# Performance work log

Hardware: AMD Instinct MI355X
Metric: run time of the kernel (lower is better)

Reference implementation:

```python
import jax, jax.numpy as jnp
import numpy as np

EMBED_DIM = 1024
NUM_HEADS = 16
FFN_DIM = 4096
N_QUBITS = 8
LN_EPS = 1e-5


def _layernorm(x, g, b):
    mu = jnp.mean(x, axis=-1, keepdims=True)
    var = jnp.mean(jnp.square(x - mu), axis=-1, keepdims=True)
    return (x - mu) * jax.lax.rsqrt(var + LN_EPS) * g + b


def setup_inputs() -> dict:
    key = jax.random.key(0)
    ks = jax.random.split(key, 12)
    E, F_, Q = EMBED_DIM, FFN_DIM, N_QUBITS
    s = 1.0 / np.sqrt(E)
    return {
        "x": jax.random.normal(ks[0], (4, 2048, E), dtype=jnp.float32),
        "wq": jax.random.normal(ks[1], (E, E), dtype=jnp.float32) * s,
        "wk": jax.random.normal(ks[2], (E, E), dtype=jnp.float32) * s,
        "wv": jax.random.normal(ks[3], (E, E), dtype=jnp.float32) * s,
        "wo": jax.random.normal(ks[4], (E, E), dtype=jnp.float32) * s,
        "theta": jax.random.normal(ks[5], (Q,), dtype=jnp.float32),
        "w1": jax.random.normal(ks[6], (Q, F_), dtype=jnp.float32) * (1.0 / np.sqrt(Q)),
        "w2": jax.random.normal(ks[7], (F_, E), dtype=jnp.float32) * (1.0 / np.sqrt(F_)),
        "ln1_g": jnp.ones((E,), dtype=jnp.float32),
        "ln1_b": jnp.zeros((E,), dtype=jnp.float32),
        "ln2_g": jnp.ones((E,), dtype=jnp.float32),
        "ln2_b": jnp.zeros((E,), dtype=jnp.float32),
    }


def reference(x, wq, wk, wv, wo, theta, w1, w2, ln1_g, ln1_b, ln2_g, ln2_b):
    B, S, E = x.shape
    H, Dk = NUM_HEADS, E // NUM_HEADS
    # ---- multi-head attention ----
    q = (x @ wq).reshape(B, S, H, Dk).transpose(0, 2, 1, 3)  # [B,H,S,Dk]
    k = (x @ wk).reshape(B, S, H, Dk).transpose(0, 2, 1, 3)
    v = (x @ wv).reshape(B, S, H, Dk).transpose(0, 2, 1, 3)
    scores = jnp.einsum("bhsd,bhtd->bhst", q, k) / np.sqrt(Dk)
    attn = jax.nn.softmax(scores, axis=-1)
    ctx = jnp.einsum("bhst,bhtd->bhsd", attn, v)
    ctx = ctx.transpose(0, 2, 1, 3).reshape(B, S, E)
    attn_out = ctx @ wo
    x1 = _layernorm(x + attn_out, ln1_g, ln1_b)
    # ---- quantum FFN ----
    # Per qubit w: |0> -> RX(x1_w) -> RX(x1_w) -> RX(theta_w); <Z> = cos(2*x1_w + theta_w)
    q_out = jnp.cos(2.0 * x1[..., :N_QUBITS] + theta)  # [B,S,Q]
    ffn_out = jax.nn.relu(q_out @ w1) @ w2  # [B,S,E]
    return _layernorm(x1 + ffn_out, ln2_g, ln2_b)
```

## Files before the change

### kernel.cpp

```cpp
#include <hip/hip_runtime.h>
#include <hip/hip_bf16.h>


typedef __attribute__((ext_vector_type(8))) short bf16x8;
typedef __attribute__((ext_vector_type(16))) float f32x16;
typedef __attribute__((ext_vector_type(4))) unsigned short u16x4;

__device__ __forceinline__ unsigned short f2bf(float f) {
  union { float f; unsigned int u; } v; v.f = f;
  return (unsigned short)((v.u + 0x7FFFu + ((v.u >> 16) & 1u)) >> 16);
}
__device__ __forceinline__ float bf2f(unsigned short h) {
  union { unsigned int u; float f; } v; v.u = ((unsigned int)h) << 16;
  return v.f;
}
__device__ __forceinline__ f32x16 mfma32(bf16x8 a, bf16x8 b, f32x16 c) {
  return __builtin_amdgcn_mfma_f32_32x32x16_bf16(a, b, c, 0, 0, 0);
}
__device__ __forceinline__ void lds_cp16(const void* g, void* l) {
  __builtin_amdgcn_global_load_lds(
      (const __attribute__((address_space(1))) unsigned int*)g,
      (__attribute__((address_space(3))) unsigned int*)l, 16, 0, 0);
}

#define QG_CONV(P, FC0, FC1)                                                  \
  {                                                                           \
    int x0a, x0b, x1a, x1b, x2a, x2b, x3a, x3b;                               \
    asm("v_cvt_pk_bf16_f32 %0, %1, %2" : "=v"(x0a) : "v"(P[0]),  "v"(P[1]));  \
    asm("v_cvt_pk_bf16_f32 %0, %1, %2" : "=v"(x0b) : "v"(P[2]),  "v"(P[3]));  \
    asm("v_cvt_pk_bf16_f32 %0, %1, %2" : "=v"(x1a) : "v"(P[4]),  "v"(P[5]));  \
    asm("v_cvt_pk_bf16_f32 %0, %1, %2" : "=v"(x1b) : "v"(P[6]),  "v"(P[7]));  \
    asm("v_cvt_pk_bf16_f32 %0, %1, %2" : "=v"(x2a) : "v"(P[8]),  "v"(P[9]));  \
    asm("v_cvt_pk_bf16_f32 %0, %1, %2" : "=v"(x2b) : "v"(P[10]), "v"(P[11])); \
    asm("v_cvt_pk_bf16_f32 %0, %1, %2" : "=v"(x3a) : "v"(P[12]), "v"(P[13])); \
    asm("v_cvt_pk_bf16_f32 %0, %1, %2" : "=v"(x3b) : "v"(P[14]), "v"(P[15])); \
    asm("v_permlane32_swap_b32 %0, %1" : "+v"(x0a), "+v"(x1a));               \
    asm("v_permlane32_swap_b32 %0, %1" : "+v"(x0b), "+v"(x1b));               \
    asm("v_permlane32_swap_b32 %0, %1" : "+v"(x2a), "+v"(x3a));               \
    asm("v_permlane32_swap_b32 %0, %1" : "+v"(x2b), "+v"(x3b));               \
    union { int u[4]; bf16x8 v; } f0_, f1_;                                   \
    f0_.u[0] = x0a; f0_.u[1] = x0b; f0_.u[2] = x1a; f0_.u[3] = x1b;           \
    f1_.u[0] = x2a; f1_.u[1] = x2b; f1_.u[2] = x3a; f1_.u[3] = x3b;           \
    FC0 = f0_.v; FC1 = f1_.v;                                                 \
  }

__global__ __launch_bounds__(256) void cast_x_kernel(const float* __restrict__ in,
                                                     unsigned short* __restrict__ out,
                                                     int n4) {
  int i = blockIdx.x * 256 + threadIdx.x;
  if (i >= n4) return;
  float4 v = ((const float4*)in)[i];
  u16x4 o = { f2bf(v.x), f2bf(v.y), f2bf(v.z), f2bf(v.w) };
  ((u16x4*)out)[i] = o;
}

__global__ __launch_bounds__(256) void transpose_cast_kernel(const float* __restrict__ in,
                                                             unsigned short* __restrict__ out,
                                                             int K, int N) {
  __shared__ float tile[32][33];
  const int n0 = blockIdx.x * 32, k0 = blockIdx.y * 32;
  const int tx = threadIdx.x, ty = threadIdx.y;
#pragma unroll
  for (int i = 0; i < 32; i += 8)
    tile[ty + i][tx] = in[(long)(k0 + ty + i) * N + n0 + tx];
  __syncthreads();
#pragma unroll
  for (int i = 0; i < 32; i += 8)
    out[(long)(n0 + ty + i) * K + k0 + tx] = f2bf(tile[tx][ty + i]);
}

__global__ __launch_bounds__(256) void w1t_kernel(const float* __restrict__ w1,
                                                  unsigned short* __restrict__ w1t) {
  const int f = blockIdx.x * 256 + threadIdx.x;
  unsigned short v[8];
#pragma unroll
  for (int q = 0; q < 8; q++) v[q] = f2bf(w1[q * 4096 + f]);
  *(u16x4*)(w1t + f * 8)     = (u16x4){v[0], v[1], v[2], v[3]};
  *(u16x4*)(w1t + f * 8 + 4) = (u16x4){v[4], v[5], v[6], v[7]};
}

__global__ __launch_bounds__(256) void vt_kernel(const unsigned short* __restrict__ qkv,
                                                 unsigned short* __restrict__ vT) {
  __shared__ unsigned short tile[32][34];
  const int t0 = blockIdx.x * 32, d0 = blockIdx.y * 32, bh = blockIdx.z;
  const int b = bh >> 4, h = bh & 15;
  const int tx = threadIdx.x, ty = threadIdx.y;
  const unsigned short* src = qkv + (long)(b * 2048 + t0) * 3072 + 2048 + h * 64 + d0;
#pragma unroll
  for (int i = 0; i < 32; i += 8)
    tile[ty + i][tx] = src[(long)(ty + i) * 3072 + tx];
  __syncthreads();
  unsigned short* dst = vT + ((long)bh * 64 + d0) * 2048 + t0;
#pragma unroll
  for (int i = 0; i < 32; i += 8)
    dst[(long)(ty + i) * 2048 + tx] = tile[tx][ty + i];
}

template<int EPI>
__global__ __launch_bounds__(256) void gemm_bt3(const unsigned short* __restrict__ A,
                                                const unsigned short* __restrict__ BT,
                                                void* __restrict__ Cv,
                                                int M, int N, int K) {
  __shared__ __align__(16) unsigned char smem[2][32768];
  const int tid = threadIdx.x;
  const int l = tid & 63, w = tid >> 6;
  const int l32 = l & 31, h32 = l >> 5;
  const int wrm = (w >> 1) * 64;
  const int wrn = (w & 1) * 64;

  const int nx = gridDim.x;
  const int nwg = nx * gridDim.y;
  const int orig = blockIdx.y * nx + blockIdx.x;
  const int chunk = nwg >> 3;
  const int logical = (orig & 7) * chunk + (orig >> 3);
  const long m0 = (long)(logical / nx) * 128;
  const long n0 = (long)(logical % nx) * 128;

  const unsigned short* gp[8];
  unsigned ldsoff[8];
#pragma unroll
  for (int i = 0; i < 8; i++) {
    const int c = (i & 3) * 256 + tid;
    const int r = c >> 3, k8 = c & 7;
    if (i < 4) {
      gp[i] = A + (m0 + r) * (long)K + (k8 ^ (r & 7)) * 8;
      ldsoff[i] = (unsigned)c * 16;
    } else {
      gp[i] = BT + (n0 + r) * (long)K + (k8 ^ (r & 7)) * 8;
      ldsoff[i] = 16384u + (unsigned)c * 16;
    }
  }

  f32x16 acc[2][2];
#pragma unroll
  for (int mf = 0; mf < 2; mf++)
#pragma unroll
    for (int nf = 0; nf < 2; nf++)
#pragma unroll
      for (int e = 0; e < 16; e++) acc[mf][nf][e] = 0.f;

  const int NT = K >> 6;
#define STAGE(bf, t)                                                    \
  do {                                                                  \
    unsigned char* _d = &smem[bf][0];                                   \
    const long _ko = (long)(t) * 64;                                    \
    _Pragma("unroll")                                                   \
    for (int _i = 0; _i < 8; _i++)                                      \
      lds_cp16(gp[_i] + _ko, _d + ldsoff[_i]);                          \
  } while (0)

  STAGE(0, 0);
  int cur = 0;
  for (int t = 0; t < NT; t++) {
    if (t + 1 < NT) {
      STAGE(cur ^ 1, t + 1);
      asm volatile("s_waitcnt vmcnt(8)" ::: "memory");
    } else {
      asm volatile("s_waitcnt vmcnt(0)" ::: "memory");
    }
    __builtin_amdgcn_sched_barrier(0);
    __builtin_amdgcn_s_barrier();
    __builtin_amdgcn_sched_barrier(0);

    const unsigned char* bufA = &smem[cur][0];
    const unsigned char* bufB = &smem[cur][16384];
    bf16x8 af[2][4], bfr[2][4];
#pragma unroll
    for (int mf = 0; mf < 2; mf++) {
      const int r = wrm + mf * 32 + l32;
#pragma unroll
      for (int ks = 0; ks < 4; ks++)
        af[mf][ks] = *(const bf16x8*)(bufA + r * 128 + (((ks * 2 + h32) ^ (r & 7)) * 16));
    }
#pragma unroll
    for (int nf = 0; nf < 2; nf++) {
      const int r = wrn + nf * 32 + l32;
#pragma unroll
      for (int ks = 0; ks < 4; ks++)
        bfr[nf][ks] = *(const bf16x8*)(bufB + r * 128 + (((ks * 2 + h32) ^ (r & 7)) * 16));
    }
    __builtin_amdgcn_s_setprio(1);
#pragma unroll
    for (int ks = 0; ks < 4; ks++)
#pragma unroll
      for (int mf = 0; mf < 2; mf++)
#pragma unroll
        for (int nf = 0; nf < 2; nf++)
          acc[mf][nf] = mfma32(af[mf][ks], bfr[nf][ks], acc[mf][nf]);
    __builtin_amdgcn_s_setprio(0);
    __builtin_amdgcn_sched_barrier(0);
    __builtin_amdgcn_s_barrier();
    cur ^= 1;
  }
#undef STAGE

#pragma unroll
  for (int mf = 0; mf < 2; mf++)
#pragma unroll
    for (int nf = 0; nf < 2; nf++) {
      const long c0 = n0 + wrn + nf * 32 + l32;
#pragma unroll
      for (int reg = 0; reg < 16; reg++) {
        const long r0 = m0 + wrm + mf * 32 + (reg & 3) + 8 * (reg >> 2) + 4 * h32;
        if (EPI == 0) ((float*)Cv)[r0 * (long)N + c0] = acc[mf][nf][reg];
        else ((unsigned short*)Cv)[r0 * (long)N + c0] = f2bf(acc[mf][nf][reg]);
      }
    }
}

__global__ __launch_bounds__(512) void ffn_fused(const unsigned short* __restrict__ qo,
                                                 const unsigned short* __restrict__ w1t,
                                                 const unsigned short* __restrict__ BT,
                                                 float* __restrict__ Cp0,
                                                 float* __restrict__ Cp1,
                                                 int N, int K) {
  __shared__ __align__(16) unsigned char sm[2 * 16384 + 32768 + 4096];
  unsigned char* lsW = sm + 32768;
  unsigned char* lsQ = sm + 65536;
  const int tid = threadIdx.x;
  const int l = tid & 63, w = tid >> 6;
  const int l32 = l & 31, h32 = l >> 5;
  const int wrm = (w >> 1) * 64;
  const int wrn = (w & 1) * 64;

  const int nx = gridDim.x;
  const int nwg = nx * gridDim.y;
  const int orig = blockIdx.y * nx + blockIdx.x;
  const int chunk = nwg >> 3;
  const int logical = (orig & 7) * chunk + (orig >> 3);
  const long m0 = (long)(logical / nx) * 256;
  const long n0 = (long)(logical % nx) * 128;
  const int kz = blockIdx.z;
  const int NT = (K >> 6) >> 1;
  const int tbase = kz * NT;
  float* C = kz ? Cp1 : Cp0;

  const unsigned short* gpB[2];
  unsigned offB[2];
#pragma unroll
  for (int i = 0; i < 2; i++) {
    const int c = i * 512 + tid;
    const int r = c >> 3, k8 = c & 7;
    gpB[i] = BT + (n0 + r) * (long)K + (long)tbase * 64 + (k8 ^ (r & 7)) * 8;
    offB[i] = (unsigned)c * 16;
  }
  const unsigned short* w1base = w1t + (long)tbase * 64 * 8;

  const bf16x8 z8 = {0, 0, 0, 0, 0, 0, 0, 0};

#define STAGE_B(bf, t)                                                  \
  do {                                                                  \
    unsigned char* _d = sm + (bf) * 16384;                              \
    const long _ko = (long)(t) * 64;                                    \
    lds_cp16(gpB[0] + _ko, _d + offB[0]);                               \
    lds_cp16(gpB[1] + _ko, _d + offB[1]);                               \
  } while (0)
#define STAGE_W1(T)                                                     \
  lds_cp16(w1base + (long)((T) * 64 + l) * 8, lsW + ((unsigned)(T) << 10))

  STAGE_W1(0);
  STAGE_W1(1);
  if (w < 4) lds_cp16(qo + (m0 + w * 64 + l) * 8, lsQ + (unsigned)(w * 64) * 16);
  STAGE_B(0, 0);
  asm volatile("s_waitcnt vmcnt(0)" ::: "memory");
  __builtin_amdgcn_s_barrier();

  bf16x8 qof[2];
#pragma unroll
  for (int mf = 0; mf < 2; mf++)
    qof[mf] = (h32 == 0) ? *(const bf16x8*)(lsQ + (wrm + mf * 32 + l32) * 16) : z8;

  f32x16 zz;
#pragma unroll
  for (int e = 0; e < 16; e++) zz[e] = 0.f;
  f32x16 acc[2][2];
#pragma unroll
  for (int mf = 0; mf < 2; mf++)
#pragma unroll
    for (int nf = 0; nf < 2; nf++) acc[mf][nf] = zz;

  f32x16 hP0, hP1;
  {
    bf16x8 wf0 = (h32 == 0) ? *(const bf16x8*)(lsW + (0 + l32) * 16) : z8;
    bf16x8 wf1 = (h32 == 0) ? *(const bf16x8*)(lsW + (32 + l32) * 16) : z8;
    hP0 = mfma32(wf0, qof[0], zz);
    hP1 = mfma32(wf1, qof[0], zz);
  }

  int cur = 0;
  for (int t = 0; t < NT; t++) {
    if (t + 2 < NT) {
      STAGE_W1(t + 2);
      STAGE_B(cur ^ 1, t + 1);
      asm volatile("s_waitcnt vmcnt(3)" ::: "memory");
    } else if (t + 1 < NT) {
      STAGE_B(cur ^ 1, t + 1);
      asm volatile("s_waitcnt vmcnt(2)" ::: "memory");
    } else {
      asm volatile("s_waitcnt vmcnt(0)" ::: "memory");
    }
    __builtin_amdgcn_sched_barrier(0);
    __builtin_amdgcn_s_barrier();
    __builtin_amdgcn_sched_barrier(0);

    bf16x8 w1ft[2], w1fn[2];
#pragma unroll
    for (int tg = 0; tg < 2; tg++) {
      w1ft[tg] = (h32 == 0)
          ? *(const bf16x8*)(lsW + ((unsigned)t << 10) + (tg * 32 + l32) * 16) : z8;
      w1fn[tg] = (h32 == 0 && t + 1 < NT)
          ? *(const bf16x8*)(lsW + ((unsigned)(t + 1) << 10) + (tg * 32 + l32) * 16) : z8;
    }
    const unsigned char* bufB = sm + cur * 16384;
    bf16x8 bfr[2][4];
#pragma unroll
    for (int nf = 0; nf < 2; nf++) {
      const int r = wrn + nf * 32 + l32;
#pragma unroll
      for (int ks = 0; ks < 4; ks++)
        bfr[nf][ks] = *(const bf16x8*)(bufB + r * 128 + (((ks * 2 + h32) ^ (r & 7)) * 16));
    }

#pragma unroll
    for (int e = 0; e < 16; e++) {
      hP0[e] = fmaxf(hP0[e], 0.f);
      hP1[e] = fmaxf(hP1[e], 0.f);
    }
    bf16x8 a0, a1, a2, a3;
    QG_CONV(hP0, a0, a1)
    QG_CONV(hP1, a2, a3)
    __builtin_amdgcn_s_setprio(1);
    f32x16 hQ0 = mfma32(w1ft[0], qof[1], zz);
    f32x16 hQ1 = mfma32(w1ft[1], qof[1], zz);
    acc[0][0] = mfma32(a0, bfr[0][0], acc[0][0]);
    acc[0][0] = mfma32(a1, bfr[0][1], acc[0][0]);
    acc[0][0] = mfma32(a2, bfr[0][2], acc[0][0]);
    acc[0][0] = mfma32(a3, bfr[0][3], acc[0][0]);
    acc[0][1] = mfma32(a0, bfr[1][0], acc[0][1]);
    acc[0][1] = mfma32(a1, bfr[1][1], acc[0][1]);
    acc[0][1] = mfma32(a2, bfr[1][2], acc[0][1]);
    acc[0][1] = mfma32(a3, bfr[1][3], acc[0][1]);
    __builtin_amdgcn_s_setprio(0);

#pragma unroll
    for (int e = 0; e < 16; e++) {
      hQ0[e] = fmaxf(hQ0[e], 0.f);
      hQ1[e] = fmaxf(hQ1[e], 0.f);
    }
    bf16x8 b0, b1, b2, b3;
    QG_CONV(hQ0, b0, b1)
    QG_CONV(hQ1, b2, b3)
    __builtin_amdgcn_s_setprio(1);
    hP0 = mfma32(w1fn[0], qof[0], zz);
    hP1 = mfma32(w1fn[1], qof[0], zz);
    acc[1][0] = mfma32(b0, bfr[0][0], acc[1][0]);
    acc[1][0] = mfma32(b1, bfr[0][1], acc[1][0]);
    acc[1][0] = mfma32(b2, bfr[0][2], acc[1][0]);
    acc[1][0] = mfma32(b3, bfr[0][3], acc[1][0]);
    acc[1][1] = mfma32(b0, bfr[1][0], acc[1][1]);
    acc[1][1] = mfma32(b1, bfr[1][1], acc[1][1]);
    acc[1][1] = mfma32(b2, bfr[1][2], acc[1][1]);
    acc[1][1] = mfma32(b3, bfr[1][3], acc[1][1]);
    __builtin_amdgcn_s_setprio(0);

    __builtin_amdgcn_sched_barrier(0);
    __builtin_amdgcn_s_barrier();
    cur ^= 1;
  }
#undef STAGE_B
#undef STAGE_W1

#pragma unroll
  for (int mf = 0; mf < 2; mf++)
#pragma unroll
    for (int nf = 0; nf < 2; nf++) {
      const long c0 = n0 + wrn + nf * 32 + l32;
#pragma unroll
      for (int reg = 0; reg < 16; reg++) {
        const long r0 = m0 + wrm + mf * 32 + (reg & 3) + 8 * (reg >> 2) + 4 * h32;
        C[r0 * (long)N + c0] = acc[mf][nf][reg];
      }
    }
}

#define QG_BLOCK(P, LIP, FC0, FC1)                                            \
  {                                                                           \
    _Pragma("unroll")                                                         \
    for (int e = 0; e < 16; e++)                                              \
      asm("v_exp_f32 %0, %1" : "=v"(P[e]) : "v"(P[e]));                       \
    float s_ = 0.f;                                                           \
    _Pragma("unroll")                                                         \
    for (int e = 0; e < 16; e++) s_ += P[e];                                  \
    LIP += s_;                                                                \
    QG_CONV(P, FC0, FC1)                                                      \
  }

__global__ __launch_bounds__(256) void attn_kernel(const unsigned short* __restrict__ qkv,
                                                   const unsigned short* __restrict__ vT,
                                                   unsigned short* __restrict__ ctx) {
  __shared__ __align__(16) unsigned short lsK[64][72];
  __shared__ __align__(16) unsigned short lsV[64][72];

  const int tid = threadIdx.x;
  const int l = tid & 63, w = tid >> 6;
  const int l32 = l & 31, h32 = l >> 5;

  const int orig = blockIdx.x;
  const int logical = (orig & 7) * 64 + (orig >> 3);
  const int s0 = (logical & 7) * 256;
  const int bh = logical >> 3;
  const int b = bh >> 4, hh = bh & 15;

  const float QSC = 0.18033688f;
  const unsigned short* qg_base = qkv + (long)(b * 2048 + s0 + w * 64) * 3072 + hh * 64;
  bf16x8 qb0[4], qb1[4];
#pragma unroll
  for (int kc = 0; kc < 4; kc++) {
    bf16x8 t0v = *(const bf16x8*)(qg_base + (long)l32 * 3072 + kc * 16 + h32 * 8);
    bf16x8 t1v = *(const bf16x8*)(qg_base + (long)(32 + l32) * 3072 + kc * 16 + h32 * 8);
#pragma unroll
    for (int j = 0; j < 8; j++) {
      t0v[j] = (short)f2bf(bf2f((unsigned short)t0v[j]) * QSC);
      t1v[j] = (short)f2bf(bf2f((unsigned short)t1v[j]) * QSC);
    }
    qb0[kc] = t0v;
    qb1[kc] = t1v;
  }

  f32x16 oacc00, oacc01, oacc10, oacc11;
#pragma unroll
  for (int e = 0; e < 16; e++) {
    oacc00[e] = 0.f; oacc01[e] = 0.f; oacc10[e] = 0.f; oacc11[e] = 0.f;
  }
  float lip0 = 0.f, lip1 = 0.f;

  const int tr = tid >> 2;
  const int tc = (tid & 3) * 16;
  const unsigned short* kbase = qkv + (long)(b * 2048) * 3072 + 1024 + hh * 64;
  const unsigned short* vbase = vT + (long)bh * 64 * 2048;

  bf16x8 k0 = *(const bf16x8*)(kbase + (long)tr * 3072 + tc);
  bf16x8 k1 = *(const bf16x8*)(kbase + (long)tr * 3072 + tc + 8);
  bf16x8 v0 = *(const bf16x8*)(vbase + (long)tr * 2048 + tc);
  bf16x8 v1 = *(const bf16x8*)(vbase + (long)tr * 2048 + tc + 8);

  for (int t0 = 0; t0 < 2048; t0 += 64) {
    __syncthreads();
    *(bf16x8*)&lsK[tr][tc]     = k0;
    *(bf16x8*)&lsK[tr][tc + 8] = k1;
    *(bf16x8*)&lsV[tr][tc]     = v0;
    *(bf16x8*)&lsV[tr][tc + 8] = v1;
    __syncthreads();
    if (t0 + 64 < 2048) {
      k0 = *(const bf16x8*)(kbase + (long)(t0 + 64 + tr) * 3072 + tc);
      k1 = *(const bf16x8*)(kbase + (long)(t0 + 64 + tr) * 3072 + tc + 8);
      v0 = *(const bf16x8*)(vbase + (long)tr * 2048 + t0 + 64 + tc);
      v1 = *(const bf16x8*)(vbase + (long)tr * 2048 + t0 + 64 + tc + 8);
    }

#pragma unroll
    for (int tg = 0; tg < 2; tg++) {
      bf16x8 kb[4];
#pragma unroll
      for (int kc = 0; kc < 4; kc++)
        kb[kc] = *(const bf16x8*)&lsK[tg * 32 + l32][kc * 16 + h32 * 8];

      f32x16 p0, p1;
#pragma unroll
      for (int e = 0; e < 16; e++) { p0[e] = 0.f; p1[e] = 0.f; }
      __builtin_amdgcn_s_setprio(1);
#pragma unroll
      for (int kc = 0; kc < 4; kc++) {
        p0 = mfma32(kb[kc], qb0[kc], p0);
        p1 = mfma32(kb[kc], qb1[kc], p1);
      }
      __builtin_amdgcn_s_setprio(0);

      bf16x8 fA0, fA1, fB0, fB1;
      QG_BLOCK(p0, lip0, fA0, fA1)
      QG_BLOCK(p1, lip1, fB0, fB1)

      bf16x8 v00 = *(const bf16x8*)&lsV[l32][tg * 32 + h32 * 8];
      bf16x8 v01 = *(const bf16x8*)&lsV[l32][tg * 32 + 16 + h32 * 8];
      bf16x8 v10 = *(const bf16x8*)&lsV[32 + l32][tg * 32 + h32 * 8];
      bf16x8 v11 = *(const bf16x8*)&lsV[32 + l32][tg * 32 + 16 + h32 * 8];

      __builtin_amdgcn_s_setprio(1);
      oacc00 = mfma32(fA0, v00, oacc00);
      oacc00 = mfma32(fA1, v01, oacc00);
      oacc01 = mfma32(fA0, v10, oacc01);
      oacc01 = mfma32(fA1, v11, oacc01);
      oacc10 = mfma32(fB0, v00, oacc10);
      oacc10 = mfma32(fB1, v01, oacc10);
      oacc11 = mfma32(fB0, v10, oacc11);
      oacc11 = mfma32(fB1, v11, oacc11);
      __builtin_amdgcn_s_setprio(0);
    }
  }

  const float li0 = lip0 + __shfl_xor(lip0, 32);
  const float li1 = lip1 + __shfl_xor(lip1, 32);
  const float inv0 = 1.f / li0;
  const float inv1 = 1.f / li1;
  const long qrow0 = (long)(b * 2048 + s0 + w * 64);
  const int dcol = hh * 64 + l32;
#define STORE_QG(OA, OB, INV, QOFF)                                           \
  _Pragma("unroll")                                                           \
  for (int reg = 0; reg < 16; reg++) {                                        \
    const int rq = (reg & 3) + 8 * (reg >> 2) + 4 * h32;                      \
    const float iv = __shfl(INV, rq);                                         \
    const long q = qrow0 + (QOFF) + rq;                                       \
    ctx[q * 1024 + dcol]      = f2bf(OA[reg] * iv);                           \
    ctx[q * 1024 + dcol + 32] = f2bf(OB[reg] * iv);                           \
  }
  STORE_QG(oacc00, oacc01, inv0, 0)
  STORE_QG(oacc10, oacc11, inv1, 32)
#undef STORE_QG
}

template<bool QO, bool THREE>
__global__ __launch_bounds__(256) void ln_kernel(const float* __restrict__ ra,
                                                 const float* __restrict__ rb,
                                                 const float* __restrict__ rc,
                                                 const float* __restrict__ g,
                                                 const float* __restrict__ bb,
                                                 float* __restrict__ out,
                                                 unsigned short* __restrict__ qo,
                                                 const float* __restrict__ theta) {
  const int row = blockIdx.x;
  const int tid = threadIdx.x;
  const long base = (long)row * 1024 + tid * 4;
  float4 a = *(const float4*)(ra + base);
  float4 bv = *(const float4*)(rb + base);
  float4 r;
  r.x = a.x + bv.x; r.y = a.y + bv.y; r.z = a.z + bv.z; r.w = a.w + bv.w;
  if constexpr (THREE) {
    float4 c = *(const float4*)(rc + base);
    r.x += c.x; r.y += c.y; r.z += c.z; r.w += c.w;
  }
  float s  = r.x + r.y + r.z + r.w;
  float ss = r.x * r.x + r.y * r.y + r.z * r.z + r.w * r.w;
  for (int off = 32; off; off >>= 1) {
    s  += __shfl_down(s, off);
    ss += __shfl_down(ss, off);
  }
  __shared__ float red[4][2];
  const int wv = tid >> 6;
  if ((tid & 63) == 0) { red[wv][0] = s; red[wv][1] = ss; }
  __syncthreads();
  s  = red[0][0] + red[1][0] + red[2][0] + red[3][0];
  ss = red[0][1] + red[1][1] + red[2][1] + red[3][1];
  const float mu  = s * (1.f / 1024.f);
  const float var = ss * (1.f / 1024.f) - mu * mu;
  const float rsv = rsqrtf(var + 1e-5f);
  float4 gv  = *(const float4*)(g + tid * 4);
  float4 bbv = *(const float4*)(bb + tid * 4);
  float4 y;
  y.x = (r.x - mu) * rsv * gv.x + bbv.x;
  y.y = (r.y - mu) * rsv * gv.y + bbv.y;
  y.z = (r.z - mu) * rsv * gv.z + bbv.z;
  y.w = (r.w - mu) * rsv * gv.w + bbv.w;
  *(float4*)(out + base) = y;
  if constexpr (QO) {
    if (tid < 2) {
      float yv[4] = {y.x, y.y, y.z, y.w};
      u16x4 o;
#pragma unroll
      for (int c = 0; c < 4; c++)
        o[c] = f2bf(__cosf(2.f * yv[c] + theta[tid * 4 + c]));
      *(u16x4*)(qo + (long)row * 8 + tid * 4) = o;
    }
  }
}

extern "C" void kernel_launch(void* const* d_in, const int* in_sizes, int n_in,
                              void* d_out, int out_size, void* d_ws, size_t ws_size,
                              hipStream_t stream) {
  const float* x     = (const float*)d_in[0];
  const float* wq    = (const float*)d_in[1];
  const float* wk    = (const float*)d_in[2];
  const float* wv    = (const float*)d_in[3];
  const float* wo    = (const float*)d_in[4];
  const float* theta = (const float*)d_in[5];
  const float* w1    = (const float*)d_in[6];
  const float* w2    = (const float*)d_in[7];
  const float* g1    = (const float*)d_in[8];
  const float* b1    = (const float*)d_in[9];
  const float* g2    = (const float*)d_in[10];
  const float* b2    = (const float*)d_in[11];
  float* out = (float*)d_out;
  char* ws = (char*)d_ws;

  const long MB = 1 << 20;
  unsigned short* xb    = (unsigned short*)(ws);
  unsigned short* wqkvT = (unsigned short*)(ws + 16 * MB);
  unsigned short* woT   = (unsigned short*)(ws + 22 * MB);
  unsigned short* w2T   = (unsigned short*)(ws + 24 * MB);
  float*          x1    = (float*)(ws + 32 * MB);
  float*          fbuf  = (float*)(ws + 64 * MB);
  unsigned short* qkv   = (unsigned short*)(ws + 96 * MB);
  float*          fbuf2 = (float*)(ws + 96 * MB);
  unsigned short* vTb   = (unsigned short*)(ws + 144 * MB);
  unsigned short* qob   = (unsigned short*)(ws + 160 * MB);
  unsigned short* w1tb  = (unsigned short*)(ws + 160 * MB + 128 * 1024);
  unsigned short* ctx   = xb;

  cast_x_kernel<<<8192, 256, 0, stream>>>(x, xb, 8192 * 1024 / 4);
  dim3 tb(32, 8);
  transpose_cast_kernel<<<dim3(32, 32), tb, 0, stream>>>(wq, wqkvT, 1024, 1024);
  transpose_cast_kernel<<<dim3(32, 32), tb, 0, stream>>>(wk, wqkvT + 1024 * 1024, 1024, 1024);
  transpose_cast_kernel<<<dim3(32, 32), tb, 0, stream>>>(wv, wqkvT + 2048 * 1024, 1024, 1024);
  transpose_cast_kernel<<<dim3(32, 32), tb, 0, stream>>>(wo, woT, 1024, 1024);
  transpose_cast_kernel<<<dim3(32, 128), tb, 0, stream>>>(w2, w2T, 4096, 1024);
  w1t_kernel<<<16, 256, 0, stream>>>(w1, w1tb);

  gemm_bt3<1><<<dim3(24, 64), 256, 0, stream>>>(xb, wqkvT, qkv, 8192, 3072, 1024);

  vt_kernel<<<dim3(64, 2, 64), tb, 0, stream>>>(qkv, vTb);

  attn_kernel<<<512, 256, 0, stream>>>(qkv, vTb, ctx);

  gemm_bt3<0><<<dim3(8, 64), 256, 0, stream>>>(ctx, woT, fbuf, 8192, 1024, 1024);

  ln_kernel<true, false><<<8192, 256, 0, stream>>>(x, fbuf, nullptr, g1, b1, x1, qob, theta);

  ffn_fused<<<dim3(8, 32, 2), 512, 0, stream>>>(qob, w1tb, w2T, fbuf, fbuf2, 1024, 4096);

  ln_kernel<false, true><<<8192, 256, 0, stream>>>(x1, fbuf, fbuf2, g2, b2, out, nullptr, nullptr);
}
```

Before: 341.7 us.

## Merge weight-prep kernels into one launch and preload all W1 tiles upfront

```diff
diff --git a/kernel.cpp b/kernel.cpp
--- a/kernel.cpp
+++ b/kernel.cpp
@@ -54,29 +54,50 @@
   ((u16x4*)out)[i] = o;
 }
 
-__global__ __launch_bounds__(256) void transpose_cast_kernel(const float* __restrict__ in,
-                                                             unsigned short* __restrict__ out,
-                                                             int K, int N) {
+__global__ __launch_bounds__(256) void prep_weights(const float* __restrict__ wq,
+                                                    const float* __restrict__ wk,
+                                                    const float* __restrict__ wv,
+                                                    const float* __restrict__ wo,
+                                                    const float* __restrict__ w2,
+                                                    const float* __restrict__ w1,
+                                                    unsigned short* __restrict__ wqkvT,
+                                                    unsigned short* __restrict__ woT,
+                                                    unsigned short* __restrict__ w2T,
+                                                    unsigned short* __restrict__ w1t) {
   __shared__ float tile[32][33];
+  const int tx = threadIdx.x, ty = threadIdx.y;
+  const int z = blockIdx.z;
+
+  if (z == 0 && blockIdx.y >= 32) {
+    if (blockIdx.y < 48) {
+      const int f = (blockIdx.y - 32) * 256 + ty * 32 + tx;
+      unsigned short v[8];
+#pragma unroll
+      for (int q = 0; q < 8; q++) v[q] = f2bf(w1[q * 4096 + f]);
+      *(u16x4*)(w1t + f * 8)     = (u16x4){v[0], v[1], v[2], v[3]};
+      *(u16x4*)(w1t + f * 8 + 4) = (u16x4){v[4], v[5], v[6], v[7]};
+    }
+    return;
+  }
+  if (z < 4 && blockIdx.y >= 32) return;
+
+  const float* src;
+  unsigned short* dst;
+  int K;
+  if (z == 4)      { src = w2; dst = w2T; K = 4096; }
+  else if (z == 0) { src = wq; dst = wqkvT; K = 1024; }
+  else if (z == 1) { src = wk; dst = wqkvT + 1024 * 1024; K = 1024; }
+  else if (z == 2) { src = wv; dst = wqkvT + 2048 * 1024; K = 1024; }
+  else             { src = wo; dst = woT; K = 1024; }
+  const int N = 1024;
   const int n0 = blockIdx.x * 32, k0 = blockIdx.y * 32;
-  const int tx = threadIdx.x, ty = threadIdx.y;
 #pragma unroll
   for (int i = 0; i < 32; i += 8)
-    tile[ty + i][tx] = in[(long)(k0 + ty + i) * N + n0 + tx];
+    tile[ty + i][tx] = src[(long)(k0 + ty + i) * N + n0 + tx];
   __syncthreads();
 #pragma unroll
   for (int i = 0; i < 32; i += 8)
-    out[(long)(n0 + ty + i) * K + k0 + tx] = f2bf(tile[tx][ty + i]);
-}
-
-__global__ __launch_bounds__(256) void w1t_kernel(const float* __restrict__ w1,
-                                                  unsigned short* __restrict__ w1t) {
-  const int f = blockIdx.x * 256 + threadIdx.x;
-  unsigned short v[8];
-#pragma unroll
-  for (int q = 0; q < 8; q++) v[q] = f2bf(w1[q * 4096 + f]);
-  *(u16x4*)(w1t + f * 8)     = (u16x4){v[0], v[1], v[2], v[3]};
-  *(u16x4*)(w1t + f * 8 + 4) = (u16x4){v[4], v[5], v[6], v[7]};
+    dst[(long)(n0 + ty + i) * K + k0 + tx] = f2bf(tile[tx][ty + i]);
 }
 
 __global__ __launch_bounds__(256) void vt_kernel(const unsigned short* __restrict__ qkv,
@@ -255,11 +276,12 @@
     lds_cp16(gpB[0] + _ko, _d + offB[0]);                               \
     lds_cp16(gpB[1] + _ko, _d + offB[1]);                               \
   } while (0)
-#define STAGE_W1(T)                                                     \
-  lds_cp16(w1base + (long)((T) * 64 + l) * 8, lsW + ((unsigned)(T) << 10))
-
-  STAGE_W1(0);
-  STAGE_W1(1);
+
+#pragma unroll
+  for (int i = 0; i < 4; i++) {
+    const int slot = i * 8 + w;
+    lds_cp16(w1base + (long)(slot * 64 + l) * 8, lsW + ((unsigned)slot << 10));
+  }
   if (w < 4) lds_cp16(qo + (m0 + w * 64 + l) * 8, lsQ + (unsigned)(w * 64) * 16);
   STAGE_B(0, 0);
   asm volatile("s_waitcnt vmcnt(0)" ::: "memory");
@@ -289,11 +311,7 @@
 
   int cur = 0;
   for (int t = 0; t < NT; t++) {
-    if (t + 2 < NT) {
-      STAGE_W1(t + 2);
-      STAGE_B(cur ^ 1, t + 1);
-      asm volatile("s_waitcnt vmcnt(3)" ::: "memory");
-    } else if (t + 1 < NT) {
+    if (t + 1 < NT) {
       STAGE_B(cur ^ 1, t + 1);
       asm volatile("s_waitcnt vmcnt(2)" ::: "memory");
     } else {
@@ -368,7 +386,6 @@
     cur ^= 1;
   }
 #undef STAGE_B
-#undef STAGE_W1
 
 #pragma unroll
   for (int mf = 0; mf < 2; mf++)
@@ -607,12 +624,8 @@
 
   cast_x_kernel<<<8192, 256, 0, stream>>>(x, xb, 8192 * 1024 / 4);
   dim3 tb(32, 8);
-  transpose_cast_kernel<<<dim3(32, 32), tb, 0, stream>>>(wq, wqkvT, 1024, 1024);
-  transpose_cast_kernel<<<dim3(32, 32), tb, 0, stream>>>(wk, wqkvT + 1024 * 1024, 1024, 1024);
-  transpose_cast_kernel<<<dim3(32, 32), tb, 0, stream>>>(wv, wqkvT + 2048 * 1024, 1024, 1024);
-  transpose_cast_kernel<<<dim3(32, 32), tb, 0, stream>>>(wo, woT, 1024, 1024);
-  transpose_cast_kernel<<<dim3(32, 128), tb, 0, stream>>>(w2, w2T, 4096, 1024);
-  w1t_kernel<<<16, 256, 0, stream>>>(w1, w1tb);
+  prep_weights<<<dim3(32, 128, 5), tb, 0, stream>>>(wq, wk, wv, wo, w2, w1,
+                                                    wqkvT, woT, w2T, w1tb);
 
   gemm_bt3<1><<<dim3(24, 64), 256, 0, stream>>>(xb, wqkvT, qkv, 8192, 3072, 1024);
 
```

New measurement: 327.5 us. 1.04x faster.
